# Kernel tuning notes

Measured on AMD Instinct MI355X. Metric: run time of the kernel, lower is better.

The kernel has to match this reference:

```python
import jax, jax.numpy as jnp
import numpy as np

B, TQ, TK = 64, 1, 2048
QD, KD, U, H = 512, 512, 1024, 8
D = U // H  # per-head dim = 128


def setup_inputs() -> dict:
    key0 = jax.random.key(0)
    k0, k1, k2, k3, k4 = jax.random.split(key0, 5)
    query = jax.random.normal(k0, (B, TQ, QD), jnp.float32)
    key = jax.random.normal(k1, (B, TK, KD), jnp.float32)
    # 1x1 Conv1d == Linear: weight [out_ch, in_ch], bias [out_ch]
    Wq = jax.random.normal(k2, (U, QD), jnp.float32) / np.sqrt(QD).astype(np.float32)
    bq = jnp.zeros((U,), jnp.float32)
    Wk = jax.random.normal(k3, (U, KD), jnp.float32) / np.sqrt(KD).astype(np.float32)
    bk = jnp.zeros((U,), jnp.float32)
    # v is generated with torch.randn every forward in the original (unlearned);
    # here it is a fixed random vector of size D (per-head units).
    v = jax.random.normal(k4, (D,), jnp.float32)
    return {"query": query, "key": key, "Wq": Wq, "bq": bq, "Wk": Wk, "bk": bk, "v": v}


def reference(query, key, Wq, bq, Wk, bk, v):
    # 1x1 conv projections (channels-last linear)
    q = jnp.einsum('btq,uq->btu', query, Wq) + bq          # [B,TQ,U]
    k = jnp.einsum('btk,uk->btu', key, Wk) + bk            # [B,TK,U]
    # split heads: torch.stack(torch.split(x, D, dim=2), dim=1) -> [B,H,T,D]
    qs = q.reshape(B, TQ, H, D).transpose(0, 2, 1, 3)      # [B,H,TQ,D]
    ks = k.reshape(B, TK, H, D).transpose(0, 2, 1, 3)      # [B,H,TK,D]
    # weight-normalized random projection vector (b is zeros, folded away)
    g = np.float32(1.0) / np.sqrt(D).astype(np.float32)
    normed_v = g * v * jax.lax.rsqrt(jnp.sum(v * v))       # [D]
    # additive score: sum_d normed_v * tanh(ks + qs)  (qs broadcasts over TK)
    add = jnp.einsum('d,bhtd->bht', normed_v, jnp.tanh(ks + qs))  # [B,H,TK]
    # F.softmax without dim on a 4D tensor -> legacy dim=1 (heads axis)
    weights = jax.nn.softmax(add[:, :, None, :], axis=1)   # [B,H,TQ,TK]
    # value = unprojected key, shared across heads
    context = jnp.einsum('bhqt,btd->bhqd', weights, key)   # [B,H,TQ,KD]
    # view(B, TQ, -1): valid because TQ == 1
    return context.reshape(B, TQ, H * KD)
```

## Files before the change

### kernel.cpp

```cpp
#include <hip/hip_runtime.h>

#define B_   64
#define TK_  2048
#define KD_  512
#define U_   1024
#define H_   8
#define D_   128
#define MT   64
#define APAD 8
#define ASTR (KD_ + APAD)

typedef float f32x4 __attribute__((ext_vector_type(4)));
typedef short short8 __attribute__((ext_vector_type(8)));

__device__ __forceinline__ short f2bf(float f) {
    unsigned u = __float_as_uint(f);
    u += 0x7fffu + ((u >> 16) & 1u);
    return (short)(u >> 16);
}
__device__ __forceinline__ float bf2f(short s) {
    return __uint_as_float(((unsigned)(unsigned short)s) << 16);
}
__device__ __forceinline__ float tanh_fast(float x) {
    float e = __builtin_amdgcn_exp2f(x * 2.885390081777927f);
    return 1.0f - 2.0f * __builtin_amdgcn_rcpf(1.0f + e);
}

__global__ void nv_kernel(const float* __restrict__ v, float* __restrict__ wsNV) {
    __shared__ float red[D_];
    int tid = threadIdx.x;
    float x = v[tid];
    red[tid] = x * x;
    __syncthreads();
    if (tid == 0) {
        float s = 0.f;
        for (int i = 0; i < D_; ++i) s += red[i];
        red[0] = rsqrtf(s) * 0.08838834764831845f;
    }
    __syncthreads();
    wsNV[tid] = x * red[0];
}

__global__ void q_kernel(const float* __restrict__ query, const float* __restrict__ Wq,
                         const float* __restrict__ bq, const float* __restrict__ bk,
                         float* __restrict__ wsQ) {
    __shared__ float qrow[KD_];
    int b = blockIdx.x, ug = blockIdx.y, tid = threadIdx.x;
    if (tid < 128) ((float4*)qrow)[tid] = ((const float4*)(query + (size_t)b * KD_))[tid];
    __syncthreads();
    int u = ug * 256 + tid;
    const float4* wq = (const float4*)(Wq + (size_t)u * KD_);
    const float4* q4 = (const float4*)qrow;
    float acc = 0.f;
#pragma unroll 8
    for (int i = 0; i < KD_ / 4; ++i) {
        float4 a = q4[i], w = wq[i];
        acc += a.x * w.x + a.y * w.y + a.z * w.z + a.w * w.w;
    }
    wsQ[(size_t)b * U_ + u] = acc + bq[u] + bk[u];
}

__global__ void swz_kernel(const float* __restrict__ Wk, short* __restrict__ wsB) {
    int g = blockIdx.x * 256 + threadIdx.x;
    int slot = g >> 6, l = g & 63;
    int ublk = slot >> 4, ks = slot & 15;
    int u = ublk * 16 + (l & 15);
    int k0 = ks * 32 + ((l >> 4) << 3);
    const float* src = Wk + (size_t)u * KD_ + k0;
    short8 o;
#pragma unroll
    for (int j = 0; j < 8; ++j) o[j] = f2bf(src[j]);
    *(short8*)(wsB + (size_t)g * 8) = o;
}

__global__ __launch_bounds__(256, 2) void attn_kernel(
    const float* __restrict__ key, const short* __restrict__ wsB,
    const float* __restrict__ wsQ, const float* __restrict__ wsNV,
    float* __restrict__ out)
{
    __shared__ short As[MT * ASTR];
    __shared__ float S[MT][H_];
    __shared__ float Wt[MT][H_];

    int bx = blockIdx.x;
    int b = bx & 63, tt = bx >> 6;
    int tid = threadIdx.x;

    const float4* src = (const float4*)(key + ((size_t)b * TK_ + (size_t)tt * MT) * KD_);
#pragma unroll 8
    for (int j = 0; j < 32; ++j) {
        int i = tid + j * 256;
        float4 v = src[i];
        int t = i >> 7, c4 = (i & 127) << 2;
        short4 h4;
        h4.x = f2bf(v.x); h4.y = f2bf(v.y); h4.z = f2bf(v.z); h4.w = f2bf(v.w);
        *(short4*)&As[t * ASTR + c4] = h4;
    }
    __syncthreads();

    int w = tid >> 6, l = tid & 63;
    int l15 = l & 15, lq = l >> 4;
    const short8* bp = (const short8*)wsB;

    for (int c = 0; c < 2; ++c) {
        int ub = c * 512 + w * 128;
        int ub16 = ub >> 4;
        int bidx = ub16 * 1024 + l;

        f32x4 acc[4][8] = {};

        short8 bc[8];
#pragma unroll
        for (int nf = 0; nf < 8; ++nf) bc[nf] = bp[bidx + nf * 1024];

#pragma unroll 1
        for (int ks = 0; ks < 16; ++ks) {
            short8 bn[8];
            if (ks < 15) {
#pragma unroll
                for (int nf = 0; nf < 8; ++nf) bn[nf] = bp[bidx + nf * 1024 + (ks + 1) * 64];
            }
            short8 a[4];
#pragma unroll
            for (int mf = 0; mf < 4; ++mf)
                a[mf] = *(const short8*)&As[(mf * 16 + l15) * ASTR + ks * 32 + (lq << 3)];
#pragma unroll
            for (int mf = 0; mf < 4; ++mf)
#pragma unroll
                for (int nf = 0; nf < 8; ++nf)
                    acc[mf][nf] = __builtin_amdgcn_mfma_f32_16x16x32_bf16(a[mf], bc[nf], acc[mf][nf], 0, 0, 0);
            if (ks < 15) {
#pragma unroll
                for (int nf = 0; nf < 8; ++nf) bc[nf] = bn[nf];
            }
        }

        float qv[8], nv[8];
#pragma unroll
        for (int nf = 0; nf < 8; ++nf) {
            int d = nf * 16 + l15;
            qv[nf] = wsQ[(size_t)b * U_ + ub + d];
            nv[nf] = wsNV[d];
        }
        int h = ub >> 7;
#pragma unroll
        for (int mf = 0; mf < 4; ++mf)
#pragma unroll
            for (int r = 0; r < 4; ++r) {
                float p = 0.f;
#pragma unroll
                for (int nf = 0; nf < 8; ++nf)
                    p += nv[nf] * tanh_fast(acc[mf][nf][r] + qv[nf]);
                p += __shfl_xor(p, 1);
                p += __shfl_xor(p, 2);
                p += __shfl_xor(p, 4);
                p += __shfl_xor(p, 8);
                if (l15 == 0) S[mf * 16 + lq * 4 + r][h] = p;
            }
    }
    __syncthreads();

    if (tid < MT) {
        float sv[H_];
        float mx = -1e30f;
#pragma unroll
        for (int h = 0; h < H_; ++h) { sv[h] = S[tid][h]; mx = fmaxf(mx, sv[h]); }
        float sum = 0.f;
#pragma unroll
        for (int h = 0; h < H_; ++h) {
            sv[h] = __builtin_amdgcn_exp2f((sv[h] - mx) * 1.4426950408889634f);
            sum += sv[h];
        }
        float inv = __builtin_amdgcn_rcpf(sum);
#pragma unroll
        for (int h = 0; h < H_; ++h) Wt[tid][h] = sv[h] * inv;
    }
    __syncthreads();

    int dg = (tid & 127) << 2;
    int hb = (tid >> 7) << 2;
    float cacc[4][4] = {};
    for (int t = 0; t < MT; ++t) {
        short4 kk = *(const short4*)&As[t * ASTR + dg];
        float k0 = bf2f(kk.x), k1 = bf2f(kk.y), k2 = bf2f(kk.z), k3 = bf2f(kk.w);
#pragma unroll
        for (int j = 0; j < 4; ++j) {
            float wt = Wt[t][hb + j];
            cacc[j][0] += wt * k0; cacc[j][1] += wt * k1;
            cacc[j][2] += wt * k2; cacc[j][3] += wt * k3;
        }
    }
    float* ob = out + (size_t)b * (H_ * KD_);
#pragma unroll
    for (int j = 0; j < 4; ++j)
#pragma unroll
        for (int d = 0; d < 4; ++d)
            atomicAdd(&ob[(hb + j) * KD_ + dg + d], cacc[j][d]);
}

extern "C" void kernel_launch(void* const* d_in, const int* in_sizes, int n_in,
                              void* d_out, int out_size, void* d_ws, size_t ws_size,
                              hipStream_t stream) {
    const float* query = (const float*)d_in[0];
    const float* key   = (const float*)d_in[1];
    const float* Wq    = (const float*)d_in[2];
    const float* bq    = (const float*)d_in[3];
    const float* Wk    = (const float*)d_in[4];
    const float* bk    = (const float*)d_in[5];
    const float* v     = (const float*)d_in[6];
    float* out = (float*)d_out;

    char* ws = (char*)d_ws;
    float* wsNV = (float*)ws;
    float* wsQ  = (float*)(ws + 4096);
    short* wsB  = (short*)(ws + 524288);

    hipMemsetAsync(d_out, 0, (size_t)out_size * sizeof(float), stream);
    nv_kernel<<<1, 128, 0, stream>>>(v, wsNV);
    q_kernel<<<dim3(64, 4), 256, 0, stream>>>(query, Wq, bq, bk, wsQ);
    swz_kernel<<<256, 256, 0, stream>>>(Wk, wsB);
    attn_kernel<<<2048, 256, 0, stream>>>(key, wsB, wsQ, wsNV, out);
}
```

Measured before the change: 577.7 us.

## Replace atomic output accumulation with per-tile partials and a reduction kernel

```diff
diff --git a/kernel.cpp b/kernel.cpp
--- a/kernel.cpp
+++ b/kernel.cpp
@@ -9,6 +9,8 @@
 #define MT   64
 #define APAD 8
 #define ASTR (KD_ + APAD)
+#define NTILE (TK_ / MT)
+#define GRID (B_ * NTILE)
 
 typedef float f32x4 __attribute__((ext_vector_type(4)));
 typedef short short8 __attribute__((ext_vector_type(8)));
@@ -73,10 +75,11 @@
     *(short8*)(wsB + (size_t)g * 8) = o;
 }
 
+template <bool ATOMIC>
 __global__ __launch_bounds__(256, 2) void attn_kernel(
     const float* __restrict__ key, const short* __restrict__ wsB,
     const float* __restrict__ wsQ, const float* __restrict__ wsNV,
-    float* __restrict__ out)
+    float* __restrict__ outp)
 {
     __shared__ short As[MT * ASTR];
     __shared__ float S[MT][H_];
@@ -190,12 +193,31 @@
             cacc[j][2] += wt * k2; cacc[j][3] += wt * k3;
         }
     }
-    float* ob = out + (size_t)b * (H_ * KD_);
-#pragma unroll
-    for (int j = 0; j < 4; ++j)
-#pragma unroll
-        for (int d = 0; d < 4; ++d)
-            atomicAdd(&ob[(hb + j) * KD_ + dg + d], cacc[j][d]);
+    if (ATOMIC) {
+        float* ob = outp + (size_t)b * (H_ * KD_);
+#pragma unroll
+        for (int j = 0; j < 4; ++j)
+#pragma unroll
+            for (int d = 0; d < 4; ++d)
+                atomicAdd(&ob[(hb + j) * KD_ + dg + d], cacc[j][d]);
+    } else {
+        float* pb = outp + (size_t)bx * (H_ * KD_);
+#pragma unroll
+        for (int j = 0; j < 4; ++j)
+            *(f32x4*)&pb[(hb + j) * KD_ + dg] = *(f32x4*)&cacc[j][0];
+    }
+}
+
+__global__ void reduce_kernel(const float* __restrict__ partial, float* __restrict__ out) {
+    int o = blockIdx.x * 256 + threadIdx.x;
+    int b = o >> 10;
+    int u4 = o & 1023;
+    const f32x4* p4 = (const f32x4*)partial;
+    f32x4 s = {0.f, 0.f, 0.f, 0.f};
+#pragma unroll 8
+    for (int tt = 0; tt < NTILE; ++tt)
+        s += p4[((size_t)(tt * 64 + b)) * 1024 + u4];
+    ((f32x4*)out)[o] = s;
 }
 
 extern "C" void kernel_launch(void* const* d_in, const int* in_sizes, int n_in,
@@ -214,10 +236,19 @@
     float* wsNV = (float*)ws;
     float* wsQ  = (float*)(ws + 4096);
     short* wsB  = (short*)(ws + 524288);
-
-    hipMemsetAsync(d_out, 0, (size_t)out_size * sizeof(float), stream);
+    float* wsP  = (float*)(ws + 2 * 1024 * 1024);
+
+    size_t need = 2 * 1024 * 1024 + (size_t)GRID * (H_ * KD_) * sizeof(float);
+
     nv_kernel<<<1, 128, 0, stream>>>(v, wsNV);
     q_kernel<<<dim3(64, 4), 256, 0, stream>>>(query, Wq, bq, bk, wsQ);
     swz_kernel<<<256, 256, 0, stream>>>(Wk, wsB);
-    attn_kernel<<<2048, 256, 0, stream>>>(key, wsB, wsQ, wsNV, out);
-}
+
+    if (ws_size >= need) {
+        attn_kernel<false><<<GRID, 256, 0, stream>>>(key, wsB, wsQ, wsNV, wsP);
+        reduce_kernel<<<256, 256, 0, stream>>>(wsP, out);
+    } else {
+        hipMemsetAsync(d_out, 0, (size_t)out_size * sizeof(float), stream);
+        attn_kernel<true><<<GRID, 256, 0, stream>>>(key, wsB, wsQ, wsNV, out);
+    }
+}
```

Result: faster. 528.9 us (-8.4%).
